# Optimization experiments

Hardware: AMD Instinct MI355X
Metric: run time of the kernel (lower is better)

## Reference

```python
import jax, jax.numpy as jnp
import numpy as np

B, T, N, C, H = 2, 8, 256, 1024, 16
HD = C // H
NEG = jnp.float32(-1e30)


def _rope_tables(n_pos, head_dim):
    half = head_dim // 2
    inv = 1.0 / (10000.0 ** (np.arange(half, dtype=np.float64) / half))
    ang = np.arange(n_pos, dtype=np.float64)[:, None] * inv[None, :]  # [S, half]
    # repeat so cos/sin pair up with interleaved (even, odd) rotate-half pairs
    cos = np.repeat(np.cos(ang), 2, axis=-1).astype(np.float32)
    sin = np.repeat(np.sin(ang), 2, axis=-1).astype(np.float32)
    return jnp.asarray(cos), jnp.asarray(sin)


def setup_inputs() -> dict:
    key = jax.random.key(0)
    k = jax.random.split(key, 6)
    img = jax.random.normal(k[0], (B, T, N, C), jnp.float32)
    cam = jax.random.normal(k[1], (B, T, C), jnp.float32)
    w_qkv = 0.02 * jax.random.normal(k[2], (C, 3 * C), jnp.float32)
    w_proj = 0.02 * jax.random.normal(k[3], (C, C), jnp.float32)
    b_proj = jnp.zeros((C,), jnp.float32)
    cos_img, sin_img = _rope_tables(T * N, HD)
    cos_cam, sin_cam = _rope_tables(T, HD)
    # frame-causal mask for cam queries over fused [cam_t, img_t] KV blocks
    kv_frame = jnp.arange(T * (N + 1)) // (N + 1)          # [T*(N+1)]
    attn_mask = (kv_frame[None, :] <= jnp.arange(T)[:, None])[None, None]  # [1,1,T,T*(N+1)] bool
    return {"img": img, "cam": cam, "w_qkv": w_qkv, "w_proj": w_proj,
            "b_proj": b_proj, "cos_img": cos_img, "sin_img": sin_img,
            "cos_cam": cos_cam, "sin_cam": sin_cam, "attn_mask": attn_mask}


def _rotate_half(x):
    xp = x.reshape(x.shape[:-1] + (-1, 2))
    return jnp.stack((-xp[..., 1], xp[..., 0]), axis=-1).reshape(x.shape)


def _apply_rope(x, cos, sin):
    # x: [B,H,S,D]; cos/sin: [S,D]
    return x * cos[None, None] + _rotate_half(x) * sin[None, None]


def _qkv(x, w_qkv, num_heads):
    b, s, c = x.shape
    hd = c // num_heads
    qkv = (x @ w_qkv).reshape(b, s, 3, num_heads, hd)
    qkv = qkv.transpose(0, 3, 2, 1, 4)  # [B,H,3,S,hd]
    return qkv[:, :, 0], qkv[:, :, 1], qkv[:, :, 2]


def _sdpa(q, k, v, mask=None):
    scale = q.shape[-1] ** -0.5
    s = jnp.einsum('bhqd,bhkd->bhqk', q, k) * scale
    if mask is not None:
        s = jnp.where(mask, s, NEG)
    a = jax.nn.softmax(s, axis=-1)
    return jnp.einsum('bhqk,bhkd->bhqd', a, v)


def reference(img, cam, w_qkv, w_proj, b_proj, cos_img, sin_img, cos_cam, sin_cam, attn_mask):
    b, t, n, c = img.shape
    hd = cos_img.shape[-1]
    h = c // hd

    q_img, k_img, v_img = _qkv(img.reshape(b, t * n, c), w_qkv, h)
    q_img = _apply_rope(q_img, cos_img, sin_img)
    k_img = _apply_rope(k_img, cos_img, sin_img)

    q_cam, k_cam, v_cam = _qkv(cam, w_qkv, h)
    q_cam = _apply_rope(q_cam, cos_cam, sin_cam)
    k_cam = _apply_rope(k_cam, cos_cam, sin_cam)

    k_img = k_img.reshape(b, h, t, n, hd)
    v_img = v_img.reshape(b, h, t, n, hd)
    k_fused = jnp.concatenate([k_cam[:, :, :, None], k_img], axis=-2).reshape(b, h, t * (n + 1), hd)
    v_fused = jnp.concatenate([v_cam[:, :, :, None], v_img], axis=-2).reshape(b, h, t * (n + 1), hd)

    x_img = _sdpa(q_img, k_fused, v_fused).transpose(0, 2, 1, 3).reshape(b, t, n, c)
    x_cam = _sdpa(q_cam, k_fused, v_fused, mask=attn_mask).transpose(0, 2, 1, 3).reshape(b, t, c)

    img_out = x_img @ w_proj + b_proj
    cam_out = x_cam @ w_proj + b_proj
    return img_out, cam_out
```

## Files before the change

kernel.cpp:

```cpp
#include <hip/hip_runtime.h>

#define T_ 8
#define N_ 256
#define C_ 1024
#define H_ 16
#define D_ 64
#define U_ 2056
#define UPAD_ 2112
#define MROWS_ 4112
#define MPAD_ 4224
#define IMG_OUT_ELEMS 4194304

typedef __attribute__((ext_vector_type(4))) float f32x4;
typedef __attribute__((ext_vector_type(8))) short s16x8;
typedef __attribute__((ext_vector_type(4))) short s16x4;

__device__ __forceinline__ short f2bf(float f) {
  union { float f; unsigned u; } a; a.f = f;
  unsigned u = a.u;
  return (short)((u + 0x7fffu + ((u >> 16) & 1u)) >> 16);
}

__device__ __forceinline__ float b2f(short s) {
  union { unsigned u; float f; } a;
  a.u = ((unsigned)(unsigned short)s) << 16;
  return a.f;
}

__device__ __forceinline__ float exp2a(float x) {
  float r; asm("v_exp_f32 %0, %1" : "=v"(r) : "v"(x)); return r;
}

__device__ __forceinline__ unsigned cvt_pk_bf16(float lo, float hi) {
  unsigned r; asm("v_cvt_pk_bf16_f32 %0, %1, %2" : "=v"(r) : "v"(lo), "v"(hi)); return r;
}

#define ASYNC_COPY16(gp, lp)                                                   \
  __builtin_amdgcn_global_load_lds((const __attribute__((address_space(1))) void*)(gp), \
                                   (__attribute__((address_space(3))) void*)(lp), 16, 0, 0)

constexpr size_t OFF_XB     = 0;
constexpr size_t OFF_WQKVT  = OFF_XB + 8650752;
constexpr size_t OFF_WPROJT = OFF_WQKVT + 6291456;
constexpr size_t OFF_Q      = OFF_WPROJT + 2097152;
constexpr size_t OFF_K      = OFF_Q + 8421376;
constexpr size_t OFF_V      = OFF_K + 8650752;
constexpr size_t OFF_VT     = OFF_V + 8650752;
constexpr size_t OFF_X      = OFF_VT + 8650752;

__global__ __launch_bounds__(256) void prep_kernel(const float* __restrict__ img,
                                                   const float* __restrict__ cam,
                                                   short* __restrict__ Xb,
                                                   const float* __restrict__ wqkv,
                                                   short* __restrict__ Wqkvt,
                                                   const float* __restrict__ wproj,
                                                   short* __restrict__ Wprojt) {
  __shared__ float tile[32][33];
  const int bid = blockIdx.x;
  if (bid < 4112) {
    int gt = bid * 256 + threadIdx.x;
    int e = gt << 2;
    int row = e >> 10, col = e & 1023;
    int b = row / U_, u = row % U_, t = u / 257, jj = u % 257;
    const float* src = jj ? (img + ((size_t)((b * 8 + t) * 256 + (jj - 1)) << 10))
                          : (cam + ((size_t)(b * 8 + t) << 10));
    float4 f = *(const float4*)(src + col);
    s16x4 o;
    o[0] = f2bf(f.x); o[1] = f2bf(f.y); o[2] = f2bf(f.z); o[3] = f2bf(f.w);
    *(s16x4*)(Xb + ((size_t)row << 10) + col) = o;
    return;
  }
  const float* in; short* out; int Cc, bx, by;
  if (bid < 4112 + 3072) {
    int i = bid - 4112; bx = i % 96; by = i / 96; in = wqkv; out = Wqkvt; Cc = 3072;
  } else {
    int i = bid - 7184; bx = i % 32; by = i / 32; in = wproj; out = Wprojt; Cc = 1024;
  }
  constexpr int R = 1024;
  int tx = threadIdx.x & 31, ty = threadIdx.x >> 5;
  int col0 = bx << 5, row0 = by << 5;
#pragma unroll
  for (int i = 0; i < 4; i++) {
    int r = ty + i * 8;
    tile[r][tx] = in[(size_t)(row0 + r) * Cc + col0 + tx];
  }
  __syncthreads();
#pragma unroll
  for (int i = 0; i < 4; i++) {
    int r = ty + i * 8;
    out[(size_t)(col0 + r) * R + row0 + tx] = f2bf(tile[tx][r]);
  }
}

template <int EPI>
__global__ __launch_bounds__(256) void gemm_kernel(
    const short* __restrict__ A, const short* __restrict__ Bt,
    const float* __restrict__ cosi, const float* __restrict__ sini,
    const float* __restrict__ cosc, const float* __restrict__ sinc,
    short* __restrict__ qb, short* __restrict__ kb, short* __restrict__ vb,
    const float* __restrict__ bias, float* __restrict__ outp) {
  constexpr int K = 1024;
  __shared__ __align__(16) short As[2][64 * 32];
  __shared__ __align__(16) short Bs[2][128 * 32];
  const int tid = threadIdx.x, w = tid >> 6, lane = tid & 63;
  const int l16 = lane & 15, quad = lane >> 4;

  int bn, bm;
  {
    const int flat = blockIdx.x;
    const int xcd = flat & 7, idx = flat >> 3;
    if constexpr (EPI == 0) { bn = xcd * 3 + idx / 66; bm = idx % 66; }
    else                    { bn = xcd;                bm = idx;       }
  }

  const f32x4 zero = {0.f, 0.f, 0.f, 0.f};
  f32x4 acc[2][4];
#pragma unroll
  for (int i = 0; i < 2; i++)
#pragma unroll
    for (int j = 0; j < 4; j++) acc[i][j] = zero;

  const int mb = (w >> 1) << 5, nb = (w & 1) << 6;

  const int srow = tid >> 2;
  const int cseg = (((tid & 3) ^ (srow & 3)) << 3);
  const short* gA = A + (size_t)(bm * 64 + srow) * K + cseg;
  const short* gB = Bt + (size_t)(bn * 128 + srow) * K + cseg;
  const int lo = tid * 16;

#define STAGE(buf, kb0)                                                        \
  do {                                                                         \
    ASYNC_COPY16(gA + (kb0), (char*)As[buf] + lo);                             \
    ASYNC_COPY16(gB + (kb0), (char*)Bs[buf] + lo);                             \
    ASYNC_COPY16(gB + (size_t)64 * K + (kb0), (char*)Bs[buf] + lo + 4096);     \
  } while (0)

  STAGE(0, 0);
  int cur = 0;
  const int gsw = (quad ^ (l16 & 3)) << 3;
  for (int kb0 = 0; kb0 < K; kb0 += 32) {
    __syncthreads();
    if (kb0 + 32 < K) STAGE(cur ^ 1, kb0 + 32);
    s16x8 af[2], bf[4];
#pragma unroll
    for (int mi = 0; mi < 2; mi++)
      af[mi] = *(const s16x8*)&As[cur][(mb + mi * 16 + l16) * 32 + gsw];
#pragma unroll
    for (int ni = 0; ni < 4; ni++)
      bf[ni] = *(const s16x8*)&Bs[cur][(nb + ni * 16 + l16) * 32 + gsw];
#pragma unroll
    for (int mi = 0; mi < 2; mi++)
#pragma unroll
      for (int ni = 0; ni < 4; ni++)
        acc[mi][ni] = __builtin_amdgcn_mfma_f32_16x16x32_bf16(af[mi], bf[ni], acc[mi][ni], 0, 0, 0);
    cur ^= 1;
  }
#undef STAGE

  if constexpr (EPI == 0) {
    const int cbase = bn * 128 + nb;
    const int which = cbase >> 10;
    const int hh = (cbase & 1023) >> 6;
#pragma unroll
    for (int mi = 0; mi < 2; mi++) {
#pragma unroll
      for (int reg = 0; reg < 4; reg++) {
        const int R = bm * 64 + mb + mi * 16 + quad * 4 + reg;
        if (R < MROWS_) {
          const int b = (R >= U_) ? 1 : 0;
          const int u = R - b * U_;
          const int t = (u - (u >> 8)) >> 8;
          const int jj = u - ((t << 8) + t);
          const int bh = b * 16 + hh;
          if (which == 2) {
#pragma unroll
            for (int ni = 0; ni < 4; ni++)
              vb[((size_t)bh * UPAD_ + u) * 64 + ni * 16 + l16] = f2bf(acc[mi][ni][reg]);
          } else {
            const float *ct, *st; int pos;
            if (jj == 0) { ct = cosc; st = sinc; pos = t; }
            else         { ct = cosi; st = sini; pos = u - t - 1; }
#pragma unroll
            for (int ni = 0; ni < 4; ni++) {
              const int d = ni * 16 + l16;
              const float val = acc[mi][ni][reg];
              const float partner = __shfl_xor(val, 1, 64);
              const float cv = ct[pos * 64 + d], sv = st[pos * 64 + d];
              float o = val * cv + ((d & 1) ? partner : -partner) * sv;
              if (which == 0) {
                o *= 0.18033688f;
                qb[((size_t)bh * U_ + u) * 64 + d] = f2bf(o);
              } else {
                kb[((size_t)bh * UPAD_ + u) * 64 + d] = f2bf(o);
              }
            }
          }
        }
      }
    }
  } else {
    const int cbase = bn * 128 + nb;
#pragma unroll
    for (int mi = 0; mi < 2; mi++) {
#pragma unroll
      for (int reg = 0; reg < 4; reg++) {
        const int R = bm * 64 + mb + mi * 16 + quad * 4 + reg;
        if (R < MROWS_) {
          const int b = (R >= U_) ? 1 : 0;
          const int u = R - b * U_;
          const int t = (u - (u >> 8)) >> 8;
          const int jj = u - ((t << 8) + t);
          size_t rowoff;
          if (jj) rowoff = (size_t)((b * 8 + t) * 256 + jj - 1) * 1024;
          else    rowoff = IMG_OUT_ELEMS + (size_t)(b * 8 + t) * 1024;
#pragma unroll
          for (int ni = 0; ni < 4; ni++) {
            const int Cg = cbase + ni * 16 + l16;
            outp[rowoff + Cg] = acc[mi][ni][reg] + bias[Cg];
          }
        }
      }
    }
  }
}

__global__ __launch_bounds__(256) void attn_kernel(const short* __restrict__ q,
                                                   const short* __restrict__ k,
                                                   const short* __restrict__ vt,
                                                   short* __restrict__ x) {
  __shared__ __align__(16) short Kt[64 * 64];
  __shared__ __align__(16) short Vt[64 * 64];
  __shared__ __align__(16) short Pt[4 * 16 * 72];
  const int tid = threadIdx.x, w = tid >> 6, lane = tid & 63;
  const int l16 = lane & 15, quad = lane >> 4;
  const int flat = blockIdx.x;
  const int slot = flat >> 3;
  const int bh = ((flat & 7) << 2) + (slot >> 5);
  const int qt = slot & 31;
  const int b = bh >> 4, h = bh & 15;

  const int g = qt * 64 + w * 16 + l16;
  const int u_q = g + (g >> 8) + 1;
  const short* qp = q + ((size_t)bh * U_ + u_q) * 64;
  const s16x8 aq0 = *(const s16x8*)(qp + quad * 8);
  const s16x8 aq1 = *(const s16x8*)(qp + 32 + quad * 8);

  const int sr = w * 8 + (lane >> 3);
  const int c8 = lane & 7;
  const short* kg = k + ((size_t)bh * UPAD_ + sr) * 64 + (c8 << 3);
  const short* vg = vt + ((size_t)bh * 64 + sr) * UPAD_ + (c8 << 3);
  const int swz = ((c8 ^ (sr & 7)) << 3);
  short* const wk0 = &Kt[sr * 64 + swz];
  short* const wk1 = &Kt[(sr + 32) * 64 + swz];
  short* const wv0 = &Vt[sr * 64 + swz];
  short* const wv1 = &Vt[(sr + 32) * 64 + swz];

  const int cK0 = (quad * 8) ^ ((l16 & 7) << 3);
  const int cK1 = (32 + quad * 8) ^ ((l16 & 7) << 3);
  short* const pw = Pt + (w * 16 + l16) * 72;

  const f32x4 zero = {0.f, 0.f, 0.f, 0.f};
  const s16x8 vones = {16256, 16256, 16256, 16256, 16256, 16256, 16256, 16256};
  float m_r = -3e38f;
  f32x4 l_acc = zero;
  f32x4 o_acc[4];
#pragma unroll
  for (int r = 0; r < 4; r++) o_acc[r] = zero;

  s16x8 rk0 = *(const s16x8*)(kg);
  s16x8 rk1 = *(const s16x8*)(kg + 2048);
  s16x8 rv0 = *(const s16x8*)(vg);
  s16x8 rv1 = *(const s16x8*)(vg + 32 * UPAD_);
  kg += 64 * 64;
  vg += 64;

  for (int kv0 = 0; kv0 < U_; kv0 += 64) {
    __syncthreads();
    *(s16x8*)wk0 = rk0;
    *(s16x8*)wk1 = rk1;
    *(s16x8*)wv0 = rv0;
    *(s16x8*)wv1 = rv1;
    __syncthreads();
    if (kv0 + 64 < U_) {
      rk0 = *(const s16x8*)(kg);
      rk1 = *(const s16x8*)(kg + 2048);
      rv0 = *(const s16x8*)(vg);
      rv1 = *(const s16x8*)(vg + 32 * UPAD_);
      kg += 64 * 64;
      vg += 64;
    }

    f32x4 sT[4];
    __builtin_amdgcn_s_setprio(1);
#pragma unroll
    for (int ni = 0; ni < 4; ni++) {
      const s16x8 b0 = *(const s16x8*)&Kt[(ni * 16 + l16) * 64 + cK0];
      const s16x8 b1 = *(const s16x8*)&Kt[(ni * 16 + l16) * 64 + cK1];
      f32x4 z = __builtin_amdgcn_mfma_f32_16x16x32_bf16(b0, aq0, zero, 0, 0, 0);
      sT[ni] = __builtin_amdgcn_mfma_f32_16x16x32_bf16(b1, aq1, z, 0, 0, 0);
    }
    __builtin_amdgcn_s_setprio(0);

    if (kv0 == 2048) {
#pragma unroll
      for (int ni = 0; ni < 4; ni++) {
        if (ni > 0 || quad >= 2) {
          sT[ni][0] = -1e30f; sT[ni][1] = -1e30f;
          sT[ni][2] = -1e30f; sT[ni][3] = -1e30f;
        }
      }
    }

    float t0 = fmaxf(fmaxf(sT[0][0], sT[0][1]), sT[0][2]);
    float t1 = fmaxf(fmaxf(sT[0][3], sT[1][0]), sT[1][1]);
    float t2 = fmaxf(fmaxf(sT[1][2], sT[1][3]), sT[2][0]);
    float t3 = fmaxf(fmaxf(sT[2][1], sT[2][2]), sT[2][3]);
    float t4 = fmaxf(fmaxf(sT[3][0], sT[3][1]), sT[3][2]);
    float mx = fmaxf(fmaxf(fmaxf(t0, t1), t2), fmaxf(fmaxf(t3, t4), sT[3][3]));
    mx = fmaxf(mx, __shfl_xor(mx, 16, 64));
    mx = fmaxf(mx, __shfl_xor(mx, 32, 64));

    if (__any(mx > m_r + 8.f)) {
      const float mnew = fmaxf(m_r, mx);
      const float al = exp2a(m_r - mnew);
      m_r = mnew;
      float aR[4];
#pragma unroll
      for (int reg = 0; reg < 4; reg++) aR[reg] = __shfl(al, quad * 4 + reg, 64);
#pragma unroll
      for (int ni = 0; ni < 4; ni++)
#pragma unroll
        for (int reg = 0; reg < 4; reg++) o_acc[ni][reg] *= aR[reg];
#pragma unroll
      for (int reg = 0; reg < 4; reg++) l_acc[reg] *= aR[reg];
    }

#pragma unroll
    for (int ni = 0; ni < 4; ni++)
#pragma unroll
      for (int reg = 0; reg < 4; reg++)
        sT[ni][reg] = exp2a(sT[ni][reg] - m_r);

#pragma unroll
    for (int ni = 0; ni < 4; ni++) {
      uint2 pk;
      pk.x = cvt_pk_bf16(sT[ni][0], sT[ni][1]);
      pk.y = cvt_pk_bf16(sT[ni][2], sT[ni][3]);
      *(uint2*)&pw[ni * 16 + quad * 4] = pk;
    }

    const s16x8 ap0 = *(const s16x8*)&pw[quad * 8];
    const s16x8 ap1 = *(const s16x8*)&pw[32 + quad * 8];
    __builtin_amdgcn_s_setprio(1);
    l_acc = __builtin_amdgcn_mfma_f32_16x16x32_bf16(ap0, vones, l_acc, 0, 0, 0);
#pragma unroll
    for (int ni = 0; ni < 4; ni++) {
      const s16x8 bv = *(const s16x8*)&Vt[(ni * 16 + l16) * 64 + cK0];
      o_acc[ni] = __builtin_amdgcn_mfma_f32_16x16x32_bf16(ap0, bv, o_acc[ni], 0, 0, 0);
    }
    l_acc = __builtin_amdgcn_mfma_f32_16x16x32_bf16(ap1, vones, l_acc, 0, 0, 0);
#pragma unroll
    for (int ni = 0; ni < 4; ni++) {
      const s16x8 bv = *(const s16x8*)&Vt[(ni * 16 + l16) * 64 + cK1];
      o_acc[ni] = __builtin_amdgcn_mfma_f32_16x16x32_bf16(ap1, bv, o_acc[ni], 0, 0, 0);
    }
    __builtin_amdgcn_s_setprio(0);
  }

  f32x4 linv;
#pragma unroll
  for (int reg = 0; reg < 4; reg++) linv[reg] = 1.f / l_acc[reg];

#pragma unroll
  for (int reg = 0; reg < 4; reg++) {
    const int go = qt * 64 + w * 16 + quad * 4 + reg;
    const int u_o = go + (go >> 8) + 1;
#pragma unroll
    for (int ni = 0; ni < 4; ni++)
      x[((size_t)(b * U_ + u_o)) * 1024 + h * 64 + ni * 16 + l16] =
          f2bf(o_acc[ni][reg] * linv[reg]);
  }
}

__global__ __launch_bounds__(256) void vtcam_kernel(const short* __restrict__ v,
                                                    short* __restrict__ vt,
                                                    const short* __restrict__ q,
                                                    const short* __restrict__ k,
                                                    short* __restrict__ x) {
  __shared__ __align__(16) char smem[16448];
  const int bid = blockIdx.x;
  const int tid = threadIdx.x;
  if (bid < 1056) {
    short (*t2)[65] = (short(*)[65])smem;
    int kt = bid % 33, bh = bid / 33;
#pragma unroll
    for (int i = 0; i < 16; i++) {
      int e = tid + i * 256; int r = e >> 6, c = e & 63;
      short vv = v[((size_t)bh * UPAD_ + kt * 64 + r) * 64 + c];
      t2[r][c] = (kt * 64 + r < U_) ? vv : (short)0;
    }
    __syncthreads();
#pragma unroll
    for (int i = 0; i < 16; i++) {
      int e = tid + i * 256; int d = e >> 6, c = e & 63;
      vt[((size_t)bh * 64 + d) * UPAD_ + kt * 64 + c] = t2[c][d];
    }
    return;
  }
  float* sb = (float*)smem;
  float* red = sb + U_;
  float (*obuf)[64] = (float(*)[64])(red + 8);
  const int i0 = bid - 1056;
  const int bh = (i0 & 7) + ((i0 >> 6) << 3);
  const int t = (i0 >> 3) & 7;
  const int b = bh >> 4, h = bh & 15;
  const int L = (t + 1) * 257;
  const int lane = tid & 63, w = tid >> 6;
  const int u_q = t * 257;

  float qf[64];
  {
    const short* qpp = q + ((size_t)bh * U_ + u_q) * 64;
#pragma unroll
    for (int i = 0; i < 8; i++) {
      const s16x8 qv = *(const s16x8*)(qpp + i * 8);
#pragma unroll
      for (int j = 0; j < 8; j++) qf[i * 8 + j] = b2f(qv[j]);
    }
  }

  float lm = -3e38f;
  for (int kv = tid; kv < L; kv += 256) {
    const short* kp = k + ((size_t)bh * UPAD_ + kv) * 64;
    float s = 0.f;
#pragma unroll
    for (int i = 0; i < 8; i++) {
      const s16x8 kvv = *(const s16x8*)(kp + i * 8);
#pragma unroll
      for (int j = 0; j < 8; j++) s += qf[i * 8 + j] * b2f(kvv[j]);
    }
    sb[kv] = s;
    lm = fmaxf(lm, s);
  }
#pragma unroll
  for (int d = 1; d < 64; d <<= 1) lm = fmaxf(lm, __shfl_xor(lm, d, 64));
  if (lane == 0) red[w] = lm;
  __syncthreads();
  const float m = fmaxf(fmaxf(red[0], red[1]), fmaxf(red[2], red[3]));

  float ls = 0.f;
  for (int kv = tid; kv < L; kv += 256) {
    const float p = exp2a(sb[kv] - m);
    sb[kv] = p;
    ls += p;
  }
#pragma unroll
  for (int d = 1; d < 64; d <<= 1) ls += __shfl_xor(ls, d, 64);
  if (lane == 0) red[4 + w] = ls;
  __syncthreads();
  const float linv = 1.f / (red[4] + red[5] + red[6] + red[7]);

  const int d0 = (tid & 7) << 3;
  const int slot = tid >> 3;
  float acc[8];
#pragma unroll
  for (int j = 0; j < 8; j++) acc[j] = 0.f;
  for (int kv = slot; kv < L; kv += 32) {
    const float p = sb[kv];
    const s16x8 vv = *(const s16x8*)(v + ((size_t)bh * UPAD_ + kv) * 64 + d0);
#pragma unroll
    for (int j = 0; j < 8; j++) acc[j] += p * b2f(vv[j]);
  }
#pragma unroll
  for (int j = 0; j < 8; j++) obuf[slot][d0 + j] = acc[j];
  __syncthreads();
  if (tid < 64) {
    float s = 0.f;
#pragma unroll
    for (int i = 0; i < 32; i++) s += obuf[i][tid];
    x[((size_t)(b * U_ + u_q)) * 1024 + h * 64 + tid] = f2bf(s * linv);
  }
}

extern "C" void kernel_launch(void* const* d_in, const int* in_sizes, int n_in,
                              void* d_out, int out_size, void* d_ws, size_t ws_size,
                              hipStream_t stream) {
  const float* img   = (const float*)d_in[0];
  const float* cam   = (const float*)d_in[1];
  const float* wqkv  = (const float*)d_in[2];
  const float* wproj = (const float*)d_in[3];
  const float* bias  = (const float*)d_in[4];
  const float* cosi  = (const float*)d_in[5];
  const float* sini  = (const float*)d_in[6];
  const float* cosc  = (const float*)d_in[7];
  const float* sinc  = (const float*)d_in[8];
  float* outp = (float*)d_out;

  char* ws = (char*)d_ws;
  short* Xb     = (short*)(ws + OFF_XB);
  short* Wqkvt  = (short*)(ws + OFF_WQKVT);
  short* Wprojt = (short*)(ws + OFF_WPROJT);
  short* qb     = (short*)(ws + OFF_Q);
  short* kb     = (short*)(ws + OFF_K);
  short* vb     = (short*)(ws + OFF_V);
  short* vtb    = (short*)(ws + OFF_VT);
  short* xb     = (short*)(ws + OFF_X);

  prep_kernel<<<8208, 256, 0, stream>>>(img, cam, Xb, wqkv, Wqkvt, wproj, Wprojt);
  gemm_kernel<0><<<1584, 256, 0, stream>>>(Xb, Wqkvt, cosi, sini, cosc, sinc,
                                           qb, kb, vb, nullptr, nullptr);
  vtcam_kernel<<<1312, 256, 0, stream>>>(vb, vtb, qb, kb, xb);
  attn_kernel<<<1024, 256, 0, stream>>>(qb, kb, vtb, xb);
  gemm_kernel<1><<<528, 256, 0, stream>>>(xb, Wprojt, nullptr, nullptr, nullptr, nullptr,
                                          nullptr, nullptr, nullptr, bias, outp);
}
```

Baseline: 266.0 us.

## Process two query tiles per attention block to reuse staged K/V tiles

```diff
diff --git a/kernel.cpp b/kernel.cpp
--- a/kernel.cpp
+++ b/kernel.cpp
@@ -230,20 +230,25 @@
                                                    short* __restrict__ x) {
   __shared__ __align__(16) short Kt[64 * 64];
   __shared__ __align__(16) short Vt[64 * 64];
-  __shared__ __align__(16) short Pt[4 * 16 * 72];
+  __shared__ __align__(16) short Pt[4 * 32 * 72];
   const int tid = threadIdx.x, w = tid >> 6, lane = tid & 63;
   const int l16 = lane & 15, quad = lane >> 4;
   const int flat = blockIdx.x;
   const int slot = flat >> 3;
-  const int bh = ((flat & 7) << 2) + (slot >> 5);
-  const int qt = slot & 31;
+  const int bh = ((flat & 7) << 2) + (slot >> 4);
+  const int qt = slot & 15;
   const int b = bh >> 4, h = bh & 15;
 
-  const int g = qt * 64 + w * 16 + l16;
-  const int u_q = g + (g >> 8) + 1;
-  const short* qp = q + ((size_t)bh * U_ + u_q) * 64;
-  const s16x8 aq0 = *(const s16x8*)(qp + quad * 8);
-  const s16x8 aq1 = *(const s16x8*)(qp + 32 + quad * 8);
+  const int gA = qt * 128 + w * 16 + l16;
+  const int gB = gA + 64;
+  const int uA = gA + (gA >> 8) + 1;
+  const int uB = gB + (gB >> 8) + 1;
+  const short* qpA = q + ((size_t)bh * U_ + uA) * 64;
+  const short* qpB = q + ((size_t)bh * U_ + uB) * 64;
+  const s16x8 aq0A = *(const s16x8*)(qpA + quad * 8);
+  const s16x8 aq1A = *(const s16x8*)(qpA + 32 + quad * 8);
+  const s16x8 aq0B = *(const s16x8*)(qpB + quad * 8);
+  const s16x8 aq1B = *(const s16x8*)(qpB + 32 + quad * 8);
 
   const int sr = w * 8 + (lane >> 3);
   const int c8 = lane & 7;
@@ -257,15 +262,16 @@
 
   const int cK0 = (quad * 8) ^ ((l16 & 7) << 3);
   const int cK1 = (32 + quad * 8) ^ ((l16 & 7) << 3);
-  short* const pw = Pt + (w * 16 + l16) * 72;
+  short* const pwA = Pt + (w * 32 + l16) * 72;
+  short* const pwB = pwA + 16 * 72;
 
   const f32x4 zero = {0.f, 0.f, 0.f, 0.f};
   const s16x8 vones = {16256, 16256, 16256, 16256, 16256, 16256, 16256, 16256};
-  float m_r = -3e38f;
-  f32x4 l_acc = zero;
-  f32x4 o_acc[4];
-#pragma unroll
-  for (int r = 0; r < 4; r++) o_acc[r] = zero;
+  float mA = -3e38f, mB = -3e38f;
+  f32x4 lA = zero, lB = zero;
+  f32x4 oA[4], oB[4];
+#pragma unroll
+  for (int r = 0; r < 4; r++) { oA[r] = zero; oB[r] = zero; }
 
   s16x8 rk0 = *(const s16x8*)(kg);
   s16x8 rk1 = *(const s16x8*)(kg + 2048);
@@ -290,14 +296,16 @@
       vg += 64;
     }
 
-    f32x4 sT[4];
+    f32x4 sTA[4], sTB[4];
     __builtin_amdgcn_s_setprio(1);
 #pragma unroll
     for (int ni = 0; ni < 4; ni++) {
       const s16x8 b0 = *(const s16x8*)&Kt[(ni * 16 + l16) * 64 + cK0];
       const s16x8 b1 = *(const s16x8*)&Kt[(ni * 16 + l16) * 64 + cK1];
-      f32x4 z = __builtin_amdgcn_mfma_f32_16x16x32_bf16(b0, aq0, zero, 0, 0, 0);
-      sT[ni] = __builtin_amdgcn_mfma_f32_16x16x32_bf16(b1, aq1, z, 0, 0, 0);
+      f32x4 zA = __builtin_amdgcn_mfma_f32_16x16x32_bf16(b0, aq0A, zero, 0, 0, 0);
+      sTA[ni] = __builtin_amdgcn_mfma_f32_16x16x32_bf16(b1, aq1A, zA, 0, 0, 0);
+      f32x4 zB = __builtin_amdgcn_mfma_f32_16x16x32_bf16(b0, aq0B, zero, 0, 0, 0);
+      sTB[ni] = __builtin_amdgcn_mfma_f32_16x16x32_bf16(b1, aq1B, zB, 0, 0, 0);
     }
     __builtin_amdgcn_s_setprio(0);
 
@@ -305,80 +313,124 @@
 #pragma unroll
       for (int ni = 0; ni < 4; ni++) {
         if (ni > 0 || quad >= 2) {
-          sT[ni][0] = -1e30f; sT[ni][1] = -1e30f;
-          sT[ni][2] = -1e30f; sT[ni][3] = -1e30f;
+#pragma unroll
+          for (int r2 = 0; r2 < 4; r2++) { sTA[ni][r2] = -1e30f; sTB[ni][r2] = -1e30f; }
         }
       }
     }
 
-    float t0 = fmaxf(fmaxf(sT[0][0], sT[0][1]), sT[0][2]);
-    float t1 = fmaxf(fmaxf(sT[0][3], sT[1][0]), sT[1][1]);
-    float t2 = fmaxf(fmaxf(sT[1][2], sT[1][3]), sT[2][0]);
-    float t3 = fmaxf(fmaxf(sT[2][1], sT[2][2]), sT[2][3]);
-    float t4 = fmaxf(fmaxf(sT[3][0], sT[3][1]), sT[3][2]);
-    float mx = fmaxf(fmaxf(fmaxf(t0, t1), t2), fmaxf(fmaxf(t3, t4), sT[3][3]));
-    mx = fmaxf(mx, __shfl_xor(mx, 16, 64));
-    mx = fmaxf(mx, __shfl_xor(mx, 32, 64));
-
-    if (__any(mx > m_r + 8.f)) {
-      const float mnew = fmaxf(m_r, mx);
-      const float al = exp2a(m_r - mnew);
-      m_r = mnew;
-      float aR[4];
-#pragma unroll
-      for (int reg = 0; reg < 4; reg++) aR[reg] = __shfl(al, quad * 4 + reg, 64);
+    {
+      float t0 = fmaxf(fmaxf(sTA[0][0], sTA[0][1]), sTA[0][2]);
+      float t1 = fmaxf(fmaxf(sTA[0][3], sTA[1][0]), sTA[1][1]);
+      float t2 = fmaxf(fmaxf(sTA[1][2], sTA[1][3]), sTA[2][0]);
+      float t3 = fmaxf(fmaxf(sTA[2][1], sTA[2][2]), sTA[2][3]);
+      float t4 = fmaxf(fmaxf(sTA[3][0], sTA[3][1]), sTA[3][2]);
+      float mx = fmaxf(fmaxf(fmaxf(t0, t1), t2), fmaxf(fmaxf(t3, t4), sTA[3][3]));
+      mx = fmaxf(mx, __shfl_xor(mx, 16, 64));
+      mx = fmaxf(mx, __shfl_xor(mx, 32, 64));
+      if (__any(mx > mA + 8.f)) {
+        const float mnew = fmaxf(mA, mx);
+        const float al = exp2a(mA - mnew);
+        mA = mnew;
+        float aR[4];
+#pragma unroll
+        for (int reg = 0; reg < 4; reg++) aR[reg] = __shfl(al, quad * 4 + reg, 64);
+#pragma unroll
+        for (int ni = 0; ni < 4; ni++)
+#pragma unroll
+          for (int reg = 0; reg < 4; reg++) oA[ni][reg] *= aR[reg];
+#pragma unroll
+        for (int reg = 0; reg < 4; reg++) lA[reg] *= aR[reg];
+      }
 #pragma unroll
       for (int ni = 0; ni < 4; ni++)
 #pragma unroll
-        for (int reg = 0; reg < 4; reg++) o_acc[ni][reg] *= aR[reg];
-#pragma unroll
-      for (int reg = 0; reg < 4; reg++) l_acc[reg] *= aR[reg];
-    }
-
-#pragma unroll
-    for (int ni = 0; ni < 4; ni++)
-#pragma unroll
-      for (int reg = 0; reg < 4; reg++)
-        sT[ni][reg] = exp2a(sT[ni][reg] - m_r);
-
-#pragma unroll
-    for (int ni = 0; ni < 4; ni++) {
-      uint2 pk;
-      pk.x = cvt_pk_bf16(sT[ni][0], sT[ni][1]);
-      pk.y = cvt_pk_bf16(sT[ni][2], sT[ni][3]);
-      *(uint2*)&pw[ni * 16 + quad * 4] = pk;
-    }
-
-    const s16x8 ap0 = *(const s16x8*)&pw[quad * 8];
-    const s16x8 ap1 = *(const s16x8*)&pw[32 + quad * 8];
+        for (int reg = 0; reg < 4; reg++) sTA[ni][reg] = exp2a(sTA[ni][reg] - mA);
+#pragma unroll
+      for (int ni = 0; ni < 4; ni++) {
+        uint2 pk;
+        pk.x = cvt_pk_bf16(sTA[ni][0], sTA[ni][1]);
+        pk.y = cvt_pk_bf16(sTA[ni][2], sTA[ni][3]);
+        *(uint2*)&pwA[ni * 16 + quad * 4] = pk;
+      }
+    }
+    {
+      float t0 = fmaxf(fmaxf(sTB[0][0], sTB[0][1]), sTB[0][2]);
+      float t1 = fmaxf(fmaxf(sTB[0][3], sTB[1][0]), sTB[1][1]);
+      float t2 = fmaxf(fmaxf(sTB[1][2], sTB[1][3]), sTB[2][0]);
+      float t3 = fmaxf(fmaxf(sTB[2][1], sTB[2][2]), sTB[2][3]);
+      float t4 = fmaxf(fmaxf(sTB[3][0], sTB[3][1]), sTB[3][2]);
+      float mx = fmaxf(fmaxf(fmaxf(t0, t1), t2), fmaxf(fmaxf(t3, t4), sTB[3][3]));
+      mx = fmaxf(mx, __shfl_xor(mx, 16, 64));
+      mx = fmaxf(mx, __shfl_xor(mx, 32, 64));
+      if (__any(mx > mB + 8.f)) {
+        const float mnew = fmaxf(mB, mx);
+        const float al = exp2a(mB - mnew);
+        mB = mnew;
+        float aR[4];
+#pragma unroll
+        for (int reg = 0; reg < 4; reg++) aR[reg] = __shfl(al, quad * 4 + reg, 64);
+#pragma unroll
+        for (int ni = 0; ni < 4; ni++)
+#pragma unroll
+          for (int reg = 0; reg < 4; reg++) oB[ni][reg] *= aR[reg];
+#pragma unroll
+        for (int reg = 0; reg < 4; reg++) lB[reg] *= aR[reg];
+      }
+#pragma unroll
+      for (int ni = 0; ni < 4; ni++)
+#pragma unroll
+        for (int reg = 0; reg < 4; reg++) sTB[ni][reg] = exp2a(sTB[ni][reg] - mB);
+#pragma unroll
+      for (int ni = 0; ni < 4; ni++) {
+        uint2 pk;
+        pk.x = cvt_pk_bf16(sTB[ni][0], sTB[ni][1]);
+        pk.y = cvt_pk_bf16(sTB[ni][2], sTB[ni][3]);
+        *(uint2*)&pwB[ni * 16 + quad * 4] = pk;
+      }
+    }
+
+    const s16x8 apA0 = *(const s16x8*)&pwA[quad * 8];
+    const s16x8 apA1 = *(const s16x8*)&pwA[32 + quad * 8];
+    const s16x8 apB0 = *(const s16x8*)&pwB[quad * 8];
+    const s16x8 apB1 = *(const s16x8*)&pwB[32 + quad * 8];
     __builtin_amdgcn_s_setprio(1);
-    l_acc = __builtin_amdgcn_mfma_f32_16x16x32_bf16(ap0, vones, l_acc, 0, 0, 0);
+    lA = __builtin_amdgcn_mfma_f32_16x16x32_bf16(apA0, vones, lA, 0, 0, 0);
+    lB = __builtin_amdgcn_mfma_f32_16x16x32_bf16(apB0, vones, lB, 0, 0, 0);
 #pragma unroll
     for (int ni = 0; ni < 4; ni++) {
       const s16x8 bv = *(const s16x8*)&Vt[(ni * 16 + l16) * 64 + cK0];
-      o_acc[ni] = __builtin_amdgcn_mfma_f32_16x16x32_bf16(ap0, bv, o_acc[ni], 0, 0, 0);
-    }
-    l_acc = __builtin_amdgcn_mfma_f32_16x16x32_bf16(ap1, vones, l_acc, 0, 0, 0);
+      oA[ni] = __builtin_amdgcn_mfma_f32_16x16x32_bf16(apA0, bv, oA[ni], 0, 0, 0);
+      oB[ni] = __builtin_amdgcn_mfma_f32_16x16x32_bf16(apB0, bv, oB[ni], 0, 0, 0);
+    }
+    lA = __builtin_amdgcn_mfma_f32_16x16x32_bf16(apA1, vones, lA, 0, 0, 0);
+    lB = __builtin_amdgcn_mfma_f32_16x16x32_bf16(apB1, vones, lB, 0, 0, 0);
 #pragma unroll
     for (int ni = 0; ni < 4; ni++) {
       const s16x8 bv = *(const s16x8*)&Vt[(ni * 16 + l16) * 64 + cK1];
-      o_acc[ni] = __builtin_amdgcn_mfma_f32_16x16x32_bf16(ap1, bv, o_acc[ni], 0, 0, 0);
+      oA[ni] = __builtin_amdgcn_mfma_f32_16x16x32_bf16(apA1, bv, oA[ni], 0, 0, 0);
+      oB[ni] = __builtin_amdgcn_mfma_f32_16x16x32_bf16(apB1, bv, oB[ni], 0, 0, 0);
     }
     __builtin_amdgcn_s_setprio(0);
   }
 
-  f32x4 linv;
-#pragma unroll
-  for (int reg = 0; reg < 4; reg++) linv[reg] = 1.f / l_acc[reg];
+  f32x4 liA, liB;
+#pragma unroll
+  for (int reg = 0; reg < 4; reg++) { liA[reg] = 1.f / lA[reg]; liB[reg] = 1.f / lB[reg]; }
 
 #pragma unroll
   for (int reg = 0; reg < 4; reg++) {
-    const int go = qt * 64 + w * 16 + quad * 4 + reg;
-    const int u_o = go + (go >> 8) + 1;
-#pragma unroll
-    for (int ni = 0; ni < 4; ni++)
-      x[((size_t)(b * U_ + u_o)) * 1024 + h * 64 + ni * 16 + l16] =
-          f2bf(o_acc[ni][reg] * linv[reg]);
+    const int goA = qt * 128 + w * 16 + quad * 4 + reg;
+    const int uoA = goA + (goA >> 8) + 1;
+    const int goB = goA + 64;
+    const int uoB = goB + (goB >> 8) + 1;
+#pragma unroll
+    for (int ni = 0; ni < 4; ni++) {
+      x[((size_t)(b * U_ + uoA)) * 1024 + h * 64 + ni * 16 + l16] =
+          f2bf(oA[ni][reg] * liA[reg]);
+      x[((size_t)(b * U_ + uoB)) * 1024 + h * 64 + ni * 16 + l16] =
+          f2bf(oB[ni][reg] * liB[reg]);
+    }
   }
 }
 
@@ -510,7 +562,7 @@
   gemm_kernel<0><<<1584, 256, 0, stream>>>(Xb, Wqkvt, cosi, sini, cosc, sinc,
                                            qb, kb, vb, nullptr, nullptr);
   vtcam_kernel<<<1312, 256, 0, stream>>>(vb, vtb, qb, kb, xb);
-  attn_kernel<<<1024, 256, 0, stream>>>(qb, kb, vtb, xb);
+  attn_kernel<<<512, 256, 0, stream>>>(qb, kb, vtb, xb);
   gemm_kernel<1><<<528, 256, 0, stream>>>(xb, Wprojt, nullptr, nullptr, nullptr, nullptr,
                                           nullptr, nullptr, nullptr, bias, outp);
 }
```

Measured after the change: 268.3 us. Within noise of the previous version (+0.9%).

## Stage 128-key KV tiles per barrier pair and swizzle P buffer in attention

Applied to the files above, without the earlier changes.

```diff
diff --git a/kernel.cpp b/kernel.cpp
--- a/kernel.cpp
+++ b/kernel.cpp
@@ -228,11 +228,12 @@
                                                    const short* __restrict__ k,
                                                    const short* __restrict__ vt,
                                                    short* __restrict__ x) {
-  __shared__ __align__(16) short Kt[64 * 64];
-  __shared__ __align__(16) short Vt[64 * 64];
-  __shared__ __align__(16) short Pt[4 * 16 * 72];
+  __shared__ __align__(16) short Kt[128 * 64];
+  __shared__ __align__(16) short Vt[64 * 128];
+  __shared__ __align__(16) short Pt[4 * 16 * 64];
   const int tid = threadIdx.x, w = tid >> 6, lane = tid & 63;
   const int l16 = lane & 15, quad = lane >> 4;
+  const int l7 = l16 & 7;
   const int flat = blockIdx.x;
   const int slot = flat >> 3;
   const int bh = ((flat & 7) << 2) + (slot >> 5);
@@ -249,15 +250,21 @@
   const int c8 = lane & 7;
   const short* kg = k + ((size_t)bh * UPAD_ + sr) * 64 + (c8 << 3);
   const short* vg = vt + ((size_t)bh * 64 + sr) * UPAD_ + (c8 << 3);
-  const int swz = ((c8 ^ (sr & 7)) << 3);
-  short* const wk0 = &Kt[sr * 64 + swz];
-  short* const wk1 = &Kt[(sr + 32) * 64 + swz];
-  short* const wv0 = &Vt[sr * 64 + swz];
-  short* const wv1 = &Vt[(sr + 32) * 64 + swz];
-
-  const int cK0 = (quad * 8) ^ ((l16 & 7) << 3);
-  const int cK1 = (32 + quad * 8) ^ ((l16 & 7) << 3);
-  short* const pw = Pt + (w * 16 + l16) * 72;
+  const int s7 = sr & 7;
+  short* const wk0 = &Kt[(sr      ) * 64 + ((c8 ^ s7) << 3)];
+  short* const wk1 = &Kt[(sr + 32 ) * 64 + ((c8 ^ s7) << 3)];
+  short* const wk2 = &Kt[(sr + 64 ) * 64 + ((c8 ^ s7) << 3)];
+  short* const wk3 = &Kt[(sr + 96 ) * 64 + ((c8 ^ s7) << 3)];
+  short* const wv00 = &Vt[(sr     ) * 128 + (((c8     ) ^ s7) << 3)];
+  short* const wv10 = &Vt[(sr + 32) * 128 + (((c8     ) ^ s7) << 3)];
+  short* const wv01 = &Vt[(sr     ) * 128 + (((c8 + 8 ) ^ s7) << 3)];
+  short* const wv11 = &Vt[(sr + 32) * 128 + (((c8 + 8 ) ^ s7) << 3)];
+
+  const int cK0 = (quad * 8) ^ (l7 << 3);
+  const int cK1 = (32 + quad * 8) ^ (l7 << 3);
+  short* const pw = Pt + (w * 16 + l16) * 64;
+  const int ql4 = (quad & 1) << 2;
+  const int qh = quad >> 1;
 
   const f32x4 zero = {0.f, 0.f, 0.f, 0.f};
   const s16x8 vones = {16256, 16256, 16256, 16256, 16256, 16256, 16256, 16256};
@@ -269,102 +276,118 @@
 
   s16x8 rk0 = *(const s16x8*)(kg);
   s16x8 rk1 = *(const s16x8*)(kg + 2048);
-  s16x8 rv0 = *(const s16x8*)(vg);
-  s16x8 rv1 = *(const s16x8*)(vg + 32 * UPAD_);
-  kg += 64 * 64;
-  vg += 64;
-
-  for (int kv0 = 0; kv0 < U_; kv0 += 64) {
+  s16x8 rk2 = *(const s16x8*)(kg + 4096);
+  s16x8 rk3 = *(const s16x8*)(kg + 6144);
+  s16x8 rv00 = *(const s16x8*)(vg);
+  s16x8 rv10 = *(const s16x8*)(vg + 32 * UPAD_);
+  s16x8 rv01 = *(const s16x8*)(vg + 64);
+  s16x8 rv11 = *(const s16x8*)(vg + 32 * UPAD_ + 64);
+  kg += 128 * 64;
+  vg += 128;
+
+  for (int kv0 = 0; kv0 < 2176; kv0 += 128) {
     __syncthreads();
-    *(s16x8*)wk0 = rk0;
-    *(s16x8*)wk1 = rk1;
-    *(s16x8*)wv0 = rv0;
-    *(s16x8*)wv1 = rv1;
+    *(s16x8*)wk0 = rk0;  *(s16x8*)wk1 = rk1;
+    *(s16x8*)wk2 = rk2;  *(s16x8*)wk3 = rk3;
+    *(s16x8*)wv00 = rv00; *(s16x8*)wv10 = rv10;
+    *(s16x8*)wv01 = rv01; *(s16x8*)wv11 = rv11;
     __syncthreads();
-    if (kv0 + 64 < U_) {
+    if (kv0 + 128 < 2176) {
       rk0 = *(const s16x8*)(kg);
       rk1 = *(const s16x8*)(kg + 2048);
-      rv0 = *(const s16x8*)(vg);
-      rv1 = *(const s16x8*)(vg + 32 * UPAD_);
-      kg += 64 * 64;
-      vg += 64;
-    }
-
-    f32x4 sT[4];
-    __builtin_amdgcn_s_setprio(1);
-#pragma unroll
-    for (int ni = 0; ni < 4; ni++) {
-      const s16x8 b0 = *(const s16x8*)&Kt[(ni * 16 + l16) * 64 + cK0];
-      const s16x8 b1 = *(const s16x8*)&Kt[(ni * 16 + l16) * 64 + cK1];
-      f32x4 z = __builtin_amdgcn_mfma_f32_16x16x32_bf16(b0, aq0, zero, 0, 0, 0);
-      sT[ni] = __builtin_amdgcn_mfma_f32_16x16x32_bf16(b1, aq1, z, 0, 0, 0);
-    }
-    __builtin_amdgcn_s_setprio(0);
-
-    if (kv0 == 2048) {
+      rk2 = *(const s16x8*)(kg + 4096);
+      rk3 = *(const s16x8*)(kg + 6144);
+      rv00 = *(const s16x8*)(vg);
+      rv10 = *(const s16x8*)(vg + 32 * UPAD_);
+      rv01 = *(const s16x8*)(vg + 64);
+      rv11 = *(const s16x8*)(vg + 32 * UPAD_ + 64);
+      kg += 128 * 64;
+      vg += 128;
+    }
+
+    for (int sub = 0; sub < 2; ++sub) {
+      const int kvs = kv0 + (sub << 6);
+      if (kvs >= 2112) break;
+      const int rbase = sub << 6;
+
+      f32x4 sT[4];
+      __builtin_amdgcn_s_setprio(1);
 #pragma unroll
       for (int ni = 0; ni < 4; ni++) {
-        if (ni > 0 || quad >= 2) {
-          sT[ni][0] = -1e30f; sT[ni][1] = -1e30f;
-          sT[ni][2] = -1e30f; sT[ni][3] = -1e30f;
+        const s16x8 b0 = *(const s16x8*)&Kt[(rbase + ni * 16 + l16) * 64 + cK0];
+        const s16x8 b1 = *(const s16x8*)&Kt[(rbase + ni * 16 + l16) * 64 + cK1];
+        f32x4 z = __builtin_amdgcn_mfma_f32_16x16x32_bf16(b0, aq0, zero, 0, 0, 0);
+        sT[ni] = __builtin_amdgcn_mfma_f32_16x16x32_bf16(b1, aq1, z, 0, 0, 0);
+      }
+      __builtin_amdgcn_s_setprio(0);
+
+      if (kvs == 2048) {
+#pragma unroll
+        for (int ni = 0; ni < 4; ni++) {
+          if (ni > 0 || quad >= 2) {
+            sT[ni][0] = -1e30f; sT[ni][1] = -1e30f;
+            sT[ni][2] = -1e30f; sT[ni][3] = -1e30f;
+          }
         }
       }
-    }
-
-    float t0 = fmaxf(fmaxf(sT[0][0], sT[0][1]), sT[0][2]);
-    float t1 = fmaxf(fmaxf(sT[0][3], sT[1][0]), sT[1][1]);
-    float t2 = fmaxf(fmaxf(sT[1][2], sT[1][3]), sT[2][0]);
-    float t3 = fmaxf(fmaxf(sT[2][1], sT[2][2]), sT[2][3]);
-    float t4 = fmaxf(fmaxf(sT[3][0], sT[3][1]), sT[3][2]);
-    float mx = fmaxf(fmaxf(fmaxf(t0, t1), t2), fmaxf(fmaxf(t3, t4), sT[3][3]));
-    mx = fmaxf(mx, __shfl_xor(mx, 16, 64));
-    mx = fmaxf(mx, __shfl_xor(mx, 32, 64));
-
-    if (__any(mx > m_r + 8.f)) {
-      const float mnew = fmaxf(m_r, mx);
-      const float al = exp2a(m_r - mnew);
-      m_r = mnew;
-      float aR[4];
-#pragma unroll
-      for (int reg = 0; reg < 4; reg++) aR[reg] = __shfl(al, quad * 4 + reg, 64);
+
+      float t0 = fmaxf(fmaxf(sT[0][0], sT[0][1]), sT[0][2]);
+      float t1 = fmaxf(fmaxf(sT[0][3], sT[1][0]), sT[1][1]);
+      float t2 = fmaxf(fmaxf(sT[1][2], sT[1][3]), sT[2][0]);
+      float t3 = fmaxf(fmaxf(sT[2][1], sT[2][2]), sT[2][3]);
+      float t4 = fmaxf(fmaxf(sT[3][0], sT[3][1]), sT[3][2]);
+      float mx = fmaxf(fmaxf(fmaxf(t0, t1), t2), fmaxf(fmaxf(t3, t4), sT[3][3]));
+      mx = fmaxf(mx, __shfl_xor(mx, 16, 64));
+      mx = fmaxf(mx, __shfl_xor(mx, 32, 64));
+
+      if (__any(mx > m_r + 8.f)) {
+        const float mnew = fmaxf(m_r, mx);
+        const float al = exp2a(m_r - mnew);
+        m_r = mnew;
+        float aR[4];
+#pragma unroll
+        for (int reg = 0; reg < 4; reg++) aR[reg] = __shfl(al, quad * 4 + reg, 64);
+#pragma unroll
+        for (int ni = 0; ni < 4; ni++)
+#pragma unroll
+          for (int reg = 0; reg < 4; reg++) o_acc[ni][reg] *= aR[reg];
+#pragma unroll
+        for (int reg = 0; reg < 4; reg++) l_acc[reg] *= aR[reg];
+      }
+
 #pragma unroll
       for (int ni = 0; ni < 4; ni++)
 #pragma unroll
-        for (int reg = 0; reg < 4; reg++) o_acc[ni][reg] *= aR[reg];
-#pragma unroll
-      for (int reg = 0; reg < 4; reg++) l_acc[reg] *= aR[reg];
-    }
-
-#pragma unroll
-    for (int ni = 0; ni < 4; ni++)
-#pragma unroll
-      for (int reg = 0; reg < 4; reg++)
-        sT[ni][reg] = exp2a(sT[ni][reg] - m_r);
-
-#pragma unroll
-    for (int ni = 0; ni < 4; ni++) {
-      uint2 pk;
-      pk.x = cvt_pk_bf16(sT[ni][0], sT[ni][1]);
-      pk.y = cvt_pk_bf16(sT[ni][2], sT[ni][3]);
-      *(uint2*)&pw[ni * 16 + quad * 4] = pk;
-    }
-
-    const s16x8 ap0 = *(const s16x8*)&pw[quad * 8];
-    const s16x8 ap1 = *(const s16x8*)&pw[32 + quad * 8];
-    __builtin_amdgcn_s_setprio(1);
-    l_acc = __builtin_amdgcn_mfma_f32_16x16x32_bf16(ap0, vones, l_acc, 0, 0, 0);
-#pragma unroll
-    for (int ni = 0; ni < 4; ni++) {
-      const s16x8 bv = *(const s16x8*)&Vt[(ni * 16 + l16) * 64 + cK0];
-      o_acc[ni] = __builtin_amdgcn_mfma_f32_16x16x32_bf16(ap0, bv, o_acc[ni], 0, 0, 0);
-    }
-    l_acc = __builtin_amdgcn_mfma_f32_16x16x32_bf16(ap1, vones, l_acc, 0, 0, 0);
-#pragma unroll
-    for (int ni = 0; ni < 4; ni++) {
-      const s16x8 bv = *(const s16x8*)&Vt[(ni * 16 + l16) * 64 + cK1];
-      o_acc[ni] = __builtin_amdgcn_mfma_f32_16x16x32_bf16(ap1, bv, o_acc[ni], 0, 0, 0);
-    }
-    __builtin_amdgcn_s_setprio(0);
+        for (int reg = 0; reg < 4; reg++)
+          sT[ni][reg] = exp2a(sT[ni][reg] - m_r);
+
+#pragma unroll
+      for (int ni = 0; ni < 4; ni++) {
+        uint2 pk;
+        pk.x = cvt_pk_bf16(sT[ni][0], sT[ni][1]);
+        pk.y = cvt_pk_bf16(sT[ni][2], sT[ni][3]);
+        *(uint2*)&pw[((((ni << 1) + qh) ^ l7) << 3) + ql4] = pk;
+      }
+
+      const s16x8 ap0 = *(const s16x8*)&pw[(quad ^ l7) << 3];
+      const s16x8 ap1 = *(const s16x8*)&pw[((4 + quad) ^ l7) << 3];
+      __builtin_amdgcn_s_setprio(1);
+      l_acc = __builtin_amdgcn_mfma_f32_16x16x32_bf16(ap0, vones, l_acc, 0, 0, 0);
+#pragma unroll
+      for (int ni = 0; ni < 4; ni++) {
+        const s16x8 bv = *(const s16x8*)&Vt[(ni * 16 + l16) * 128 +
+                                           (((rbase >> 3) + quad) ^ l7) * 8];
+        o_acc[ni] = __builtin_amdgcn_mfma_f32_16x16x32_bf16(ap0, bv, o_acc[ni], 0, 0, 0);
+      }
+      l_acc = __builtin_amdgcn_mfma_f32_16x16x32_bf16(ap1, vones, l_acc, 0, 0, 0);
+#pragma unroll
+      for (int ni = 0; ni < 4; ni++) {
+        const s16x8 bv = *(const s16x8*)&Vt[(ni * 16 + l16) * 128 +
+                                           (((rbase >> 3) + 4 + quad) ^ l7) * 8];
+        o_acc[ni] = __builtin_amdgcn_mfma_f32_16x16x32_bf16(ap1, bv, o_acc[ni], 0, 0, 0);
+      }
+      __builtin_amdgcn_s_setprio(0);
+    }
   }
 
   f32x4 linv;
```

Result: slower. 275.7 us (+3.7%).
